# Kernel tuning notes

Hardware: AMD Instinct MI355X
Metric: run time of the kernel (lower is better)

## Reference

```python
import jax, jax.numpy as jnp
import numpy as np

B, T, N, F = 4, 12, 4096, 32
NG = 14  # 14 gate GNNs: fx,fh,ix,ih,cx,ch,ox,oh,i,im,g,gm,o,om


def setup_inputs() -> dict:
    key = jax.random.key(0)
    k1, k2, k3 = jax.random.split(key, 3)
    x = jax.random.normal(k1, (B, T, N, F), dtype=jnp.float32)
    # weighted adjacency, scaled like row-normalized so adj@x stays O(1)
    adj = jax.random.uniform(k2, (B, N, N), dtype=jnp.float32) / N
    W = jax.random.normal(k3, (NG, F, 2 * F), dtype=jnp.float32) * (1.0 / np.sqrt(F))
    b = jnp.zeros((NG, 2 * F), dtype=jnp.float32)
    return {"x": x, "adj": adj, "W": W, "b": b}


def _wgc(v, adj, Wi, bi):
    # WeightedGraphConv: adj-matmul -> Dense(2F) -> GLU
    y = jnp.matmul(adj, v)                 # [B,N,F]
    z = jnp.matmul(y, Wi) + bi             # [B,N,2F]
    ls, rs = jnp.split(z, 2, axis=-1)
    return ls * jax.nn.sigmoid(rs)         # [B,N,F]


def reference(x, adj, W, b):
    Bb, Tt, Nn, Ff = x.shape
    ones = jnp.ones((Bb, Nn, Ff), dtype=x.dtype)
    h0, c0, m0 = ones, ones, ones

    def step(carry, xt):
        h, c, m = carry
        g = lambda i, v: _wgc(v, adj, W[i], b[i])
        f = jax.nn.sigmoid(g(0, xt) + g(1, h))     # forget
        i = jax.nn.sigmoid(g(2, xt) + g(3, h))     # input
        o = jax.nn.sigmoid(g(6, xt) + g(7, h))     # output
        c_new = f * c + i * jnp.tanh(g(4, xt) + g(5, h))
        h_mid = o * jnp.tanh(c_new)
        # memory-state gates (has_memory_state=True)
        i2 = jax.nn.sigmoid(g(8, h_mid) + g(9, m))
        gg = jax.nn.sigmoid(g(10, h_mid) + g(11, m))
        o2 = jax.nn.sigmoid(g(12, h_mid) + g(13, m))
        m_new = i2 * m + (1.0 - i2) * gg
        h_new = m_new * o2
        return (h_new, c_new, m_new), h_new

    (last_h, last_c, last_m), hs = jax.lax.scan(step, (h0, c0, m0), jnp.swapaxes(x, 0, 1))
    hidden_states = jnp.swapaxes(hs, 0, 1)  # [B,T,N,F]
    return hidden_states, last_h, last_c, last_m
```

## Files before the change

kernel.cpp:

```cpp
#include <hip/hip_runtime.h>


typedef __bf16 bf16_t;
typedef __bf16 bf16x8 __attribute__((ext_vector_type(8)));
typedef float  f32x4  __attribute__((ext_vector_type(4)));

#define DI __device__ __forceinline__

#define BB 4
#define TT 12
#define NN 4096
#define FF 32

DI float sigm(float x)  { return __builtin_amdgcn_rcpf(1.f + __expf(-x)); }
DI float tanh_f(float x){ float e = __expf(2.f * x); return 1.f - 2.f * __builtin_amdgcn_rcpf(e + 1.f); }

__global__ __launch_bounds__(256) void conv_adj_k(const float* __restrict__ a,
                                                  bf16_t* __restrict__ o) {
    size_t i = ((size_t)blockIdx.x * 256 + threadIdx.x) * 8;
    float4 v0 = *(const float4*)(a + i);
    float4 v1 = *(const float4*)(a + i + 4);
    union { uint4 u; bf16_t h[8]; } t;
    t.h[0] = (bf16_t)v0.x; t.h[1] = (bf16_t)v0.y; t.h[2] = (bf16_t)v0.z; t.h[3] = (bf16_t)v0.w;
    t.h[4] = (bf16_t)v1.x; t.h[5] = (bf16_t)v1.y; t.h[6] = (bf16_t)v1.z; t.h[7] = (bf16_t)v1.w;
    *(uint4*)(o + i) = t.u;
}

__global__ __launch_bounds__(256) void xpose_k(const float* __restrict__ x,
                                               bf16_t* __restrict__ xT) {
    const int b = blockIdx.z, t = blockIdx.y, n0 = blockIdx.x * 64;
    const int tid = threadIdx.x;
    __shared__ float tile[64][33];
    const float* src = x + (((size_t)(b * TT + t)) * NN + n0) * FF;
#pragma unroll
    for (int rr = 0; rr < 2; ++rr) {
        int idx = rr * 256 + tid;
        int row = idx >> 3, seg = idx & 7;
        float4 v = *(const float4*)(src + row * FF + seg * 4);
        tile[row][seg * 4 + 0] = v.x; tile[row][seg * 4 + 1] = v.y;
        tile[row][seg * 4 + 2] = v.z; tile[row][seg * 4 + 3] = v.w;
    }
    __syncthreads();
    const int f = tid >> 3, seg = tid & 7;
    union { uint4 u; bf16_t h[8]; } o;
#pragma unroll
    for (int j = 0; j < 8; ++j) o.h[j] = (bf16_t)tile[seg * 8 + j][f];
    *(uint4*)&xT[((size_t)(b * 384 + t * FF + f)) * NN + n0 + seg * 8] = o.u;
}

__global__ __launch_bounds__(256) void make_wfrag_k(const float* __restrict__ W,
                                                    bf16_t* __restrict__ Wf) {
    const int g = blockIdx.x, tid = threadIdx.x;
    const int ct = tid >> 6, lane = tid & 63;
    const int k0 = (lane >> 4) * 8, col = ct * 16 + (lane & 15);
    union { uint4 u; bf16_t h[8]; } t;
#pragma unroll
    for (int j = 0; j < 8; ++j) t.h[j] = (bf16_t)W[(g * 32 + k0 + j) * 64 + col];
    *(uint4*)&Wf[((g * 4 + ct) * 64 + lane) * 8] = t.u;
}

__global__ __launch_bounds__(256) void init_k(bf16_t* h_bf, bf16_t* hm_bf,
                                              float* c, float* m,
                                              float* Y1, float* Y2) {
    const int idx = blockIdx.x * 256 + threadIdx.x;
    Y1[idx] = 0.f;
    Y2[idx] = 0.f;
    if (idx < 524288) {
        const int b = idx >> 17, r = idx & 131071;
        h_bf[idx] = (bf16_t)1.f;
        hm_bf[(size_t)b * 262144 + 131072 + r] = (bf16_t)1.f;
        c[idx] = 1.f;
        m[idx] = 1.f;
    }
}

template <bool ABF, int S, int BS0, int BS1>
__global__ __launch_bounds__(256, 4) void gemm_splitk(const void* __restrict__ Ap,
                                                      const bf16_t* __restrict__ p0,
                                                      const bf16_t* __restrict__ p1,
                                                      float* __restrict__ Y) {
    const int b = blockIdx.z;
    const int row0 = blockIdx.x * 64;
    const int slice = blockIdx.y;
    const int tid = threadIdx.x, wave = tid >> 6, lane = tid & 63;
    const int mrow = lane & 15, quad = lane >> 4;
    __shared__ __align__(16) bf16_t Vs[64 * 256];
    const f32x4 zero = {0.f, 0.f, 0.f, 0.f};
    f32x4 acc[4];
#pragma unroll
    for (int i = 0; i < 4; ++i) acc[i] = zero;
    const int row = row0 + wave * 16 + mrow;
    const size_t arow = ((size_t)b << 24) + (size_t)row * NN;

    for (int stg = 0; stg < 4; ++stg) {
        const int k0 = slice * 1024 + stg * 256;
        bf16x8 af[8];
        if constexpr (ABF) {
            const bf16_t* ab = (const bf16_t*)Ap + arow + k0 + quad * 8;
#pragma unroll
            for (int s = 0; s < 8; ++s) af[s] = *(const bf16x8*)(ab + s * 32);
        } else {
            const float* ab = (const float*)Ap + arow + k0 + quad * 8;
#pragma unroll
            for (int s = 0; s < 8; ++s) {
                float4 v0 = *(const float4*)(ab + s * 32);
                float4 v1 = *(const float4*)(ab + s * 32 + 4);
                af[s][0] = (bf16_t)v0.x; af[s][1] = (bf16_t)v0.y;
                af[s][2] = (bf16_t)v0.z; af[s][3] = (bf16_t)v0.w;
                af[s][4] = (bf16_t)v1.x; af[s][5] = (bf16_t)v1.y;
                af[s][6] = (bf16_t)v1.z; af[s][7] = (bf16_t)v1.w;
            }
        }
#pragma unroll
        for (int rr = 0; rr < 8; ++rr) {
            const int idx = rr * 256 + tid;
            const int c = idx >> 5, ch = idx & 31;
            const bf16_t* src = (S < 64 && c >= S)
                ? p1 + ((size_t)b * BS1 + (c - S)) * NN
                : p0 + ((size_t)b * BS0 + c) * NN;
            *(uint4*)&Vs[c * 256 + (ch ^ (c & 7)) * 8] =
                *(const uint4*)(src + k0 + ch * 8);
        }
        __syncthreads();
#pragma unroll
        for (int s = 0; s < 8; ++s) {
#pragma unroll
            for (int ct = 0; ct < 4; ++ct) {
                const int c = ct * 16 + mrow;
                bf16x8 bfr = *(const bf16x8*)&Vs[c * 256 + (((s * 4 + quad) ^ (c & 7)) * 8)];
                acc[ct] = __builtin_amdgcn_mfma_f32_16x16x32_bf16(af[s], bfr, acc[ct], 0, 0, 0);
            }
        }
        __syncthreads();
    }
#pragma unroll
    for (int ct = 0; ct < 4; ++ct) {
        const int col = ct * 16 + mrow;
#pragma unroll
        for (int r = 0; r < 4; ++r) {
            const int orow = row0 + wave * 16 + quad * 4 + r;
            unsafeAtomicAdd(&Y[((size_t)b * NN + orow) * 64 + col], acc[ct][r]);
        }
    }
}

__global__ __launch_bounds__(256) void gates1_k(float* __restrict__ Y1,
                                                const bf16_t* __restrict__ Wf,
                                                const float* __restrict__ bias,
                                                float* __restrict__ c,
                                                bf16_t* __restrict__ hm_bf) {
    const int b = blockIdx.y, n0 = blockIdx.x * 64;
    const int tid = threadIdx.x, wave = tid >> 6, lane = tid & 63;
    const int mrow = lane & 15, quad = lane >> 4;
    const int nw = n0 + wave * 16;
    const f32x4 zero = {0.f, 0.f, 0.f, 0.f};
    float* yr = Y1 + ((size_t)b * NN + nw + mrow) * 64;
    float4 h0 = *(float4*)(yr + quad * 8);
    float4 h1 = *(float4*)(yr + quad * 8 + 4);
    float4 x0 = *(float4*)(yr + 32 + quad * 8);
    float4 x1 = *(float4*)(yr + 32 + quad * 8 + 4);
    const float4 z4 = {0.f, 0.f, 0.f, 0.f};
    *(float4*)(yr + quad * 8) = z4;      *(float4*)(yr + quad * 8 + 4) = z4;
    *(float4*)(yr + 32 + quad * 8) = z4; *(float4*)(yr + 32 + quad * 8 + 4) = z4;
    bf16x8 ah, ax;
    ah[0] = (bf16_t)h0.x; ah[1] = (bf16_t)h0.y; ah[2] = (bf16_t)h0.z; ah[3] = (bf16_t)h0.w;
    ah[4] = (bf16_t)h1.x; ah[5] = (bf16_t)h1.y; ah[6] = (bf16_t)h1.z; ah[7] = (bf16_t)h1.w;
    ax[0] = (bf16_t)x0.x; ax[1] = (bf16_t)x0.y; ax[2] = (bf16_t)x0.z; ax[3] = (bf16_t)x0.w;
    ax[4] = (bf16_t)x1.x; ax[5] = (bf16_t)x1.y; ax[6] = (bf16_t)x1.z; ax[7] = (bf16_t)x1.w;
    float gate[4][2][4];
#pragma unroll
    for (int gi = 0; gi < 4; ++gi) {
        const int ge = 2 * gi, go = ge + 1;
        f32x4 ze[4], zo[4];
#pragma unroll
        for (int ct = 0; ct < 4; ++ct) {
            bf16x8 we = *(const bf16x8*)&Wf[((ge * 4 + ct) * 64 + lane) * 8];
            bf16x8 wo = *(const bf16x8*)&Wf[((go * 4 + ct) * 64 + lane) * 8];
            ze[ct] = __builtin_amdgcn_mfma_f32_16x16x32_bf16(ax, we, zero, 0, 0, 0);
            zo[ct] = __builtin_amdgcn_mfma_f32_16x16x32_bf16(ah, wo, zero, 0, 0, 0);
            const float be = bias[ge * 64 + ct * 16 + mrow];
            const float bo = bias[go * 64 + ct * 16 + mrow];
#pragma unroll
            for (int r = 0; r < 4; ++r) { ze[ct][r] += be; zo[ct][r] += bo; }
        }
#pragma unroll
        for (int p = 0; p < 2; ++p)
#pragma unroll
            for (int r = 0; r < 4; ++r) {
                float s = ze[p][r] * sigm(ze[p + 2][r]) + zo[p][r] * sigm(zo[p + 2][r]);
                gate[gi][p][r] = (gi == 2) ? tanh_f(s) : sigm(s);
            }
    }
    __shared__ bf16_t hmT[32][64];
#pragma unroll
    for (int p = 0; p < 2; ++p)
#pragma unroll
        for (int r = 0; r < 4; ++r) {
            const int row = nw + quad * 4 + r, col = p * 16 + mrow;
            const size_t ci = ((size_t)b * NN + row) * FF + col;
            float cn = gate[0][p][r] * c[ci] + gate[1][p][r] * gate[2][p][r];
            c[ci] = cn;
            hmT[col][wave * 16 + quad * 4 + r] = (bf16_t)(gate[3][p][r] * tanh_f(cn));
        }
    __syncthreads();
    {
        const int col = tid >> 3, seg = tid & 7;
        union { uint4 u; bf16_t h[8]; } o;
#pragma unroll
        for (int j = 0; j < 8; ++j) o.h[j] = hmT[col][seg * 8 + j];
        *(uint4*)&hm_bf[((size_t)b * 64 + col) * NN + n0 + seg * 8] = o.u;
    }
}

__global__ __launch_bounds__(256) void gates2_k(float* __restrict__ Y2,
                                                const bf16_t* __restrict__ Wf,
                                                const float* __restrict__ bias,
                                                float* __restrict__ m,
                                                bf16_t* __restrict__ hm_bf,
                                                bf16_t* __restrict__ h_bf,
                                                float* __restrict__ hs, int t) {
    const int b = blockIdx.y, n0 = blockIdx.x * 64;
    const int tid = threadIdx.x, wave = tid >> 6, lane = tid & 63;
    const int mrow = lane & 15, quad = lane >> 4;
    const int nw = n0 + wave * 16;
    const f32x4 zero = {0.f, 0.f, 0.f, 0.f};
    float* yr = Y2 + ((size_t)b * NN + nw + mrow) * 64;
    float4 h0 = *(float4*)(yr + quad * 8);
    float4 h1 = *(float4*)(yr + quad * 8 + 4);
    float4 m0 = *(float4*)(yr + 32 + quad * 8);
    float4 m1 = *(float4*)(yr + 32 + quad * 8 + 4);
    const float4 z4 = {0.f, 0.f, 0.f, 0.f};
    *(float4*)(yr + quad * 8) = z4;      *(float4*)(yr + quad * 8 + 4) = z4;
    *(float4*)(yr + 32 + quad * 8) = z4; *(float4*)(yr + 32 + quad * 8 + 4) = z4;
    bf16x8 axh, axm;
    axh[0] = (bf16_t)h0.x; axh[1] = (bf16_t)h0.y; axh[2] = (bf16_t)h0.z; axh[3] = (bf16_t)h0.w;
    axh[4] = (bf16_t)h1.x; axh[5] = (bf16_t)h1.y; axh[6] = (bf16_t)h1.z; axh[7] = (bf16_t)h1.w;
    axm[0] = (bf16_t)m0.x; axm[1] = (bf16_t)m0.y; axm[2] = (bf16_t)m0.z; axm[3] = (bf16_t)m0.w;
    axm[4] = (bf16_t)m1.x; axm[5] = (bf16_t)m1.y; axm[6] = (bf16_t)m1.z; axm[7] = (bf16_t)m1.w;
    float gate[3][2][4];
#pragma unroll
    for (int gi = 0; gi < 3; ++gi) {
        const int ge = 8 + 2 * gi, go = ge + 1;
        f32x4 ze[4], zo[4];
#pragma unroll
        for (int ct = 0; ct < 4; ++ct) {
            bf16x8 we = *(const bf16x8*)&Wf[((ge * 4 + ct) * 64 + lane) * 8];
            bf16x8 wo = *(const bf16x8*)&Wf[((go * 4 + ct) * 64 + lane) * 8];
            ze[ct] = __builtin_amdgcn_mfma_f32_16x16x32_bf16(axh, we, zero, 0, 0, 0);
            zo[ct] = __builtin_amdgcn_mfma_f32_16x16x32_bf16(axm, wo, zero, 0, 0, 0);
            const float be = bias[ge * 64 + ct * 16 + mrow];
            const float bo = bias[go * 64 + ct * 16 + mrow];
#pragma unroll
            for (int r = 0; r < 4; ++r) { ze[ct][r] += be; zo[ct][r] += bo; }
        }
#pragma unroll
        for (int p = 0; p < 2; ++p)
#pragma unroll
            for (int r = 0; r < 4; ++r) {
                float s = ze[p][r] * sigm(ze[p + 2][r]) + zo[p][r] * sigm(zo[p + 2][r]);
                gate[gi][p][r] = sigm(s);
            }
    }
    __shared__ bf16_t mT[32][64];
    __shared__ bf16_t hT[32][64];
#pragma unroll
    for (int p = 0; p < 2; ++p)
#pragma unroll
        for (int r = 0; r < 4; ++r) {
            const int row = nw + quad * 4 + r, col = p * 16 + mrow;
            const size_t ci = ((size_t)b * NN + row) * FF + col;
            const float i2 = gate[0][p][r], gg = gate[1][p][r], o2 = gate[2][p][r];
            float mn = i2 * m[ci] + (1.f - i2) * gg;
            m[ci] = mn;
            float hn = mn * o2;
            hs[(((size_t)b * TT + t) * NN + row) * FF + col] = hn;
            mT[col][wave * 16 + quad * 4 + r] = (bf16_t)mn;
            hT[col][wave * 16 + quad * 4 + r] = (bf16_t)hn;
        }
    __syncthreads();
    {
        const int col = tid >> 3, seg = tid & 7;
        union { uint4 u; bf16_t h[8]; } om, oh;
#pragma unroll
        for (int j = 0; j < 8; ++j) { om.h[j] = mT[col][seg * 8 + j]; oh.h[j] = hT[col][seg * 8 + j]; }
        *(uint4*)&hm_bf[((size_t)b * 64 + 32 + col) * NN + n0 + seg * 8] = om.u;
        *(uint4*)&h_bf[((size_t)b * FF + col) * NN + n0 + seg * 8] = oh.u;
    }
}

__global__ __launch_bounds__(256) void finalize_k(const float* __restrict__ hs,
                                                  const float* __restrict__ c,
                                                  const float* __restrict__ m,
                                                  float* __restrict__ tail) {
    const int idx = blockIdx.x * 256 + threadIdx.x;
    const int b = idx >> 17, r = idx & 131071;
    tail[idx] = hs[((size_t)b * TT + (TT - 1)) * 131072 + r];
    tail[524288 + idx] = c[idx];
    tail[1048576 + idx] = m[idx];
}

extern "C" void kernel_launch(void* const* d_in, const int* in_sizes, int n_in,
                              void* d_out, int out_size, void* d_ws, size_t ws_size,
                              hipStream_t stream) {
    const float* x    = (const float*)d_in[0];
    const float* adj  = (const float*)d_in[1];
    const float* W    = (const float*)d_in[2];
    const float* bias = (const float*)d_in[3];
    float* out = (float*)d_out;

    char* ws = (char*)d_ws;
    size_t off = 0;
    auto carve = [&](size_t bytes) -> void* {
        void* p = ws + off;
        off += (bytes + 255) & ~(size_t)255;
        return p;
    };
    bf16_t* xT    = (bf16_t*)carve((size_t)BB * 384 * NN * 2);
    float*  Y1    = (float*)carve((size_t)BB * NN * 64 * 4);
    float*  Y2    = (float*)carve((size_t)BB * NN * 64 * 4);
    bf16_t* h_bf  = (bf16_t*)carve((size_t)BB * FF * NN * 2);
    bf16_t* hm_bf = (bf16_t*)carve((size_t)BB * 64 * NN * 2);
    bf16_t* Wf    = (bf16_t*)carve((size_t)14 * 4 * 64 * 8 * 2);
    float*  cbuf  = (float*)carve((size_t)BB * NN * FF * 4);
    float*  mbuf  = (float*)carve((size_t)BB * NN * FF * 4);
    const size_t adj_bytes = (size_t)BB * NN * NN * 2;
    const bool abf = (ws_size >= off + adj_bytes);
    bf16_t* adj_bf = abf ? (bf16_t*)carve(adj_bytes) : nullptr;

    if (abf) conv_adj_k<<<32768, 256, 0, stream>>>(adj, adj_bf);
    make_wfrag_k<<<14, 256, 0, stream>>>(W, Wf);
    xpose_k<<<dim3(64, TT, BB), 256, 0, stream>>>(x, xT);
    init_k<<<4096, 256, 0, stream>>>(h_bf, hm_bf, cbuf, mbuf, Y1, Y2);

    const dim3 ggrid(64, 4, BB);
    for (int t = 0; t < TT; ++t) {
        const bf16_t* xts = xT + (size_t)t * 32 * NN;
        if (abf) gemm_splitk<true, 32, 32, 384><<<ggrid, 256, 0, stream>>>(adj_bf, h_bf, xts, Y1);
        else     gemm_splitk<false, 32, 32, 384><<<ggrid, 256, 0, stream>>>(adj, h_bf, xts, Y1);
        gates1_k<<<dim3(64, BB), 256, 0, stream>>>(Y1, Wf, bias, cbuf, hm_bf);
        if (abf) gemm_splitk<true, 64, 64, 64><<<ggrid, 256, 0, stream>>>(adj_bf, hm_bf, hm_bf, Y2);
        else     gemm_splitk<false, 64, 64, 64><<<ggrid, 256, 0, stream>>>(adj, hm_bf, hm_bf, Y2);
        gates2_k<<<dim3(64, BB), 256, 0, stream>>>(Y2, Wf, bias, mbuf, hm_bf, h_bf, out, t);
    }
    finalize_k<<<2048, 256, 0, stream>>>(out, cbuf, mbuf, out + (size_t)BB * TT * NN * FF);
}
```

Before: 1.413 ms.

## Replace atomic split-K reduction with per-slice partials and direct global B loads

The split-K GEMM no longer stages the B operand through shared memory with barriers. Each lane now loads its B fragments directly from global memory, and each K-slice writes its partial result to its own buffer instead of issuing atomic adds. The gate kernels sum the four partials on read, so the per-step zeroing of Y and the init-time clears are dropped. The adj conversion also uses nontemporal loads. The trade is 4x larger Y buffers plus extra partial reads, and B fragments that are re-read from global/L2 by every wave rather than shared through LDS.

```diff
diff --git a/kernel.cpp b/kernel.cpp
--- a/kernel.cpp
+++ b/kernel.cpp
@@ -18,11 +18,11 @@
 __global__ __launch_bounds__(256) void conv_adj_k(const float* __restrict__ a,
                                                   bf16_t* __restrict__ o) {
     size_t i = ((size_t)blockIdx.x * 256 + threadIdx.x) * 8;
-    float4 v0 = *(const float4*)(a + i);
-    float4 v1 = *(const float4*)(a + i + 4);
+    f32x4 v0 = __builtin_nontemporal_load((const f32x4*)(a + i));
+    f32x4 v1 = __builtin_nontemporal_load((const f32x4*)(a + i + 4));
     union { uint4 u; bf16_t h[8]; } t;
-    t.h[0] = (bf16_t)v0.x; t.h[1] = (bf16_t)v0.y; t.h[2] = (bf16_t)v0.z; t.h[3] = (bf16_t)v0.w;
-    t.h[4] = (bf16_t)v1.x; t.h[5] = (bf16_t)v1.y; t.h[6] = (bf16_t)v1.z; t.h[7] = (bf16_t)v1.w;
+#pragma unroll
+    for (int j = 0; j < 4; ++j) { t.h[j] = (bf16_t)v0[j]; t.h[4 + j] = (bf16_t)v1[j]; }
     *(uint4*)(o + i) = t.u;
 }
 
@@ -60,91 +60,71 @@
 }
 
 __global__ __launch_bounds__(256) void init_k(bf16_t* h_bf, bf16_t* hm_bf,
-                                              float* c, float* m,
-                                              float* Y1, float* Y2) {
+                                              float* c, float* m) {
     const int idx = blockIdx.x * 256 + threadIdx.x;
-    Y1[idx] = 0.f;
-    Y2[idx] = 0.f;
-    if (idx < 524288) {
-        const int b = idx >> 17, r = idx & 131071;
-        h_bf[idx] = (bf16_t)1.f;
-        hm_bf[(size_t)b * 262144 + 131072 + r] = (bf16_t)1.f;
-        c[idx] = 1.f;
-        m[idx] = 1.f;
-    }
+    const int b = idx >> 17, r = idx & 131071;
+    h_bf[idx] = (bf16_t)1.f;
+    hm_bf[(size_t)b * 262144 + 131072 + r] = (bf16_t)1.f;
+    c[idx] = 1.f;
+    m[idx] = 1.f;
 }
 
 template <bool ABF, int S, int BS0, int BS1>
-__global__ __launch_bounds__(256, 4) void gemm_splitk(const void* __restrict__ Ap,
+__global__ __launch_bounds__(256, 4) void gemm_direct(const void* __restrict__ Ap,
                                                       const bf16_t* __restrict__ p0,
                                                       const bf16_t* __restrict__ p1,
-                                                      float* __restrict__ Y) {
-    const int b = blockIdx.z;
+                                                      float* __restrict__ Yp) {
+    const int b = blockIdx.z, slice = blockIdx.y;
     const int row0 = blockIdx.x * 64;
-    const int slice = blockIdx.y;
     const int tid = threadIdx.x, wave = tid >> 6, lane = tid & 63;
     const int mrow = lane & 15, quad = lane >> 4;
-    __shared__ __align__(16) bf16_t Vs[64 * 256];
-    const f32x4 zero = {0.f, 0.f, 0.f, 0.f};
-    f32x4 acc[4];
-#pragma unroll
-    for (int i = 0; i < 4; ++i) acc[i] = zero;
     const int row = row0 + wave * 16 + mrow;
-    const size_t arow = ((size_t)b << 24) + (size_t)row * NN;
-
-    for (int stg = 0; stg < 4; ++stg) {
-        const int k0 = slice * 1024 + stg * 256;
-        bf16x8 af[8];
-        if constexpr (ABF) {
-            const bf16_t* ab = (const bf16_t*)Ap + arow + k0 + quad * 8;
-#pragma unroll
-            for (int s = 0; s < 8; ++s) af[s] = *(const bf16x8*)(ab + s * 32);
-        } else {
-            const float* ab = (const float*)Ap + arow + k0 + quad * 8;
-#pragma unroll
-            for (int s = 0; s < 8; ++s) {
-                float4 v0 = *(const float4*)(ab + s * 32);
-                float4 v1 = *(const float4*)(ab + s * 32 + 4);
-                af[s][0] = (bf16_t)v0.x; af[s][1] = (bf16_t)v0.y;
-                af[s][2] = (bf16_t)v0.z; af[s][3] = (bf16_t)v0.w;
-                af[s][4] = (bf16_t)v1.x; af[s][5] = (bf16_t)v1.y;
-                af[s][6] = (bf16_t)v1.z; af[s][7] = (bf16_t)v1.w;
-            }
-        }
-#pragma unroll
-        for (int rr = 0; rr < 8; ++rr) {
-            const int idx = rr * 256 + tid;
-            const int c = idx >> 5, ch = idx & 31;
-            const bf16_t* src = (S < 64 && c >= S)
-                ? p1 + ((size_t)b * BS1 + (c - S)) * NN
-                : p0 + ((size_t)b * BS0 + c) * NN;
-            *(uint4*)&Vs[c * 256 + (ch ^ (c & 7)) * 8] =
-                *(const uint4*)(src + k0 + ch * 8);
-        }
-        __syncthreads();
-#pragma unroll
-        for (int s = 0; s < 8; ++s) {
-#pragma unroll
-            for (int ct = 0; ct < 4; ++ct) {
-                const int c = ct * 16 + mrow;
-                bf16x8 bfr = *(const bf16x8*)&Vs[c * 256 + (((s * 4 + quad) ^ (c & 7)) * 8)];
-                acc[ct] = __builtin_amdgcn_mfma_f32_16x16x32_bf16(af[s], bfr, acc[ct], 0, 0, 0);
-            }
-        }
-        __syncthreads();
-    }
+    const int k0 = slice * 1024 + quad * 8;
+    const bf16_t* bp[4];
 #pragma unroll
     for (int ct = 0; ct < 4; ++ct) {
         const int col = ct * 16 + mrow;
-#pragma unroll
-        for (int r = 0; r < 4; ++r) {
-            const int orow = row0 + wave * 16 + quad * 4 + r;
-            unsafeAtomicAdd(&Y[((size_t)b * NN + orow) * 64 + col], acc[ct][r]);
-        }
-    }
-}
-
-__global__ __launch_bounds__(256) void gates1_k(float* __restrict__ Y1,
+        bp[ct] = (ct * 16 < S ? p0 + ((size_t)b * BS0 + col) * NN
+                              : p1 + ((size_t)b * BS1 + (col - S)) * NN) + k0;
+    }
+    const f32x4 zero = {0.f, 0.f, 0.f, 0.f};
+    f32x4 acc[4] = {zero, zero, zero, zero};
+    if constexpr (ABF) {
+        const bf16_t* ap = (const bf16_t*)Ap + ((size_t)b << 24) + (size_t)row * NN + k0;
+#pragma unroll 4
+        for (int kk = 0; kk < 32; ++kk) {
+            bf16x8 af = *(const bf16x8*)(ap + kk * 32);
+#pragma unroll
+            for (int ct = 0; ct < 4; ++ct) {
+                bf16x8 bfr = *(const bf16x8*)(bp[ct] + kk * 32);
+                acc[ct] = __builtin_amdgcn_mfma_f32_16x16x32_bf16(af, bfr, acc[ct], 0, 0, 0);
+            }
+        }
+    } else {
+        const float* ap = (const float*)Ap + ((size_t)b << 24) + (size_t)row * NN + k0;
+#pragma unroll 4
+        for (int kk = 0; kk < 32; ++kk) {
+            f32x4 v0 = *(const f32x4*)(ap + kk * 32);
+            f32x4 v1 = *(const f32x4*)(ap + kk * 32 + 4);
+            bf16x8 af;
+#pragma unroll
+            for (int j = 0; j < 4; ++j) { af[j] = (bf16_t)v0[j]; af[4 + j] = (bf16_t)v1[j]; }
+#pragma unroll
+            for (int ct = 0; ct < 4; ++ct) {
+                bf16x8 bfr = *(const bf16x8*)(bp[ct] + kk * 32);
+                acc[ct] = __builtin_amdgcn_mfma_f32_16x16x32_bf16(af, bfr, acc[ct], 0, 0, 0);
+            }
+        }
+    }
+    float* yb = Yp + (((size_t)b * 4 + slice) * NN + row0 + wave * 16 + quad * 4) * 64 + mrow;
+#pragma unroll
+    for (int ct = 0; ct < 4; ++ct)
+#pragma unroll
+        for (int r = 0; r < 4; ++r)
+            yb[(size_t)r * 64 + ct * 16] = acc[ct][r];
+}
+
+__global__ __launch_bounds__(256) void gates1_k(const float* __restrict__ Y1,
                                                 const bf16_t* __restrict__ Wf,
                                                 const float* __restrict__ bias,
                                                 float* __restrict__ c,
@@ -154,19 +134,22 @@
     const int mrow = lane & 15, quad = lane >> 4;
     const int nw = n0 + wave * 16;
     const f32x4 zero = {0.f, 0.f, 0.f, 0.f};
-    float* yr = Y1 + ((size_t)b * NN + nw + mrow) * 64;
-    float4 h0 = *(float4*)(yr + quad * 8);
-    float4 h1 = *(float4*)(yr + quad * 8 + 4);
-    float4 x0 = *(float4*)(yr + 32 + quad * 8);
-    float4 x1 = *(float4*)(yr + 32 + quad * 8 + 4);
-    const float4 z4 = {0.f, 0.f, 0.f, 0.f};
-    *(float4*)(yr + quad * 8) = z4;      *(float4*)(yr + quad * 8 + 4) = z4;
-    *(float4*)(yr + 32 + quad * 8) = z4; *(float4*)(yr + 32 + quad * 8 + 4) = z4;
+    const float* yr = Y1 + (((size_t)b * 4) * NN + nw + mrow) * 64 + quad * 8;
+    f32x4 h0 = zero, h1 = zero, x0 = zero, x1 = zero;
+#pragma unroll
+    for (int s = 0; s < 4; ++s) {
+        const float* p = yr + (size_t)s * NN * 64;
+        h0 += *(const f32x4*)(p);
+        h1 += *(const f32x4*)(p + 4);
+        x0 += *(const f32x4*)(p + 32);
+        x1 += *(const f32x4*)(p + 36);
+    }
     bf16x8 ah, ax;
-    ah[0] = (bf16_t)h0.x; ah[1] = (bf16_t)h0.y; ah[2] = (bf16_t)h0.z; ah[3] = (bf16_t)h0.w;
-    ah[4] = (bf16_t)h1.x; ah[5] = (bf16_t)h1.y; ah[6] = (bf16_t)h1.z; ah[7] = (bf16_t)h1.w;
-    ax[0] = (bf16_t)x0.x; ax[1] = (bf16_t)x0.y; ax[2] = (bf16_t)x0.z; ax[3] = (bf16_t)x0.w;
-    ax[4] = (bf16_t)x1.x; ax[5] = (bf16_t)x1.y; ax[6] = (bf16_t)x1.z; ax[7] = (bf16_t)x1.w;
+#pragma unroll
+    for (int j = 0; j < 4; ++j) {
+        ah[j] = (bf16_t)h0[j]; ah[4 + j] = (bf16_t)h1[j];
+        ax[j] = (bf16_t)x0[j]; ax[4 + j] = (bf16_t)x1[j];
+    }
     float gate[4][2][4];
 #pragma unroll
     for (int gi = 0; gi < 4; ++gi) {
@@ -212,7 +195,7 @@
     }
 }
 
-__global__ __launch_bounds__(256) void gates2_k(float* __restrict__ Y2,
+__global__ __launch_bounds__(256) void gates2_k(const float* __restrict__ Y2,
                                                 const bf16_t* __restrict__ Wf,
                                                 const float* __restrict__ bias,
                                                 float* __restrict__ m,
@@ -224,19 +207,22 @@
     const int mrow = lane & 15, quad = lane >> 4;
     const int nw = n0 + wave * 16;
     const f32x4 zero = {0.f, 0.f, 0.f, 0.f};
-    float* yr = Y2 + ((size_t)b * NN + nw + mrow) * 64;
-    float4 h0 = *(float4*)(yr + quad * 8);
-    float4 h1 = *(float4*)(yr + quad * 8 + 4);
-    float4 m0 = *(float4*)(yr + 32 + quad * 8);
-    float4 m1 = *(float4*)(yr + 32 + quad * 8 + 4);
-    const float4 z4 = {0.f, 0.f, 0.f, 0.f};
-    *(float4*)(yr + quad * 8) = z4;      *(float4*)(yr + quad * 8 + 4) = z4;
-    *(float4*)(yr + 32 + quad * 8) = z4; *(float4*)(yr + 32 + quad * 8 + 4) = z4;
+    const float* yr = Y2 + (((size_t)b * 4) * NN + nw + mrow) * 64 + quad * 8;
+    f32x4 h0 = zero, h1 = zero, m0 = zero, m1 = zero;
+#pragma unroll
+    for (int s = 0; s < 4; ++s) {
+        const float* p = yr + (size_t)s * NN * 64;
+        h0 += *(const f32x4*)(p);
+        h1 += *(const f32x4*)(p + 4);
+        m0 += *(const f32x4*)(p + 32);
+        m1 += *(const f32x4*)(p + 36);
+    }
     bf16x8 axh, axm;
-    axh[0] = (bf16_t)h0.x; axh[1] = (bf16_t)h0.y; axh[2] = (bf16_t)h0.z; axh[3] = (bf16_t)h0.w;
-    axh[4] = (bf16_t)h1.x; axh[5] = (bf16_t)h1.y; axh[6] = (bf16_t)h1.z; axh[7] = (bf16_t)h1.w;
-    axm[0] = (bf16_t)m0.x; axm[1] = (bf16_t)m0.y; axm[2] = (bf16_t)m0.z; axm[3] = (bf16_t)m0.w;
-    axm[4] = (bf16_t)m1.x; axm[5] = (bf16_t)m1.y; axm[6] = (bf16_t)m1.z; axm[7] = (bf16_t)m1.w;
+#pragma unroll
+    for (int j = 0; j < 4; ++j) {
+        axh[j] = (bf16_t)h0[j]; axh[4 + j] = (bf16_t)h1[j];
+        axm[j] = (bf16_t)m0[j]; axm[4 + j] = (bf16_t)m1[j];
+    }
     float gate[3][2][4];
 #pragma unroll
     for (int gi = 0; gi < 3; ++gi) {
@@ -316,8 +302,8 @@
         return p;
     };
     bf16_t* xT    = (bf16_t*)carve((size_t)BB * 384 * NN * 2);
-    float*  Y1    = (float*)carve((size_t)BB * NN * 64 * 4);
-    float*  Y2    = (float*)carve((size_t)BB * NN * 64 * 4);
+    float*  Y1    = (float*)carve((size_t)BB * 4 * NN * 64 * 4);
+    float*  Y2    = (float*)carve((size_t)BB * 4 * NN * 64 * 4);
     bf16_t* h_bf  = (bf16_t*)carve((size_t)BB * FF * NN * 2);
     bf16_t* hm_bf = (bf16_t*)carve((size_t)BB * 64 * NN * 2);
     bf16_t* Wf    = (bf16_t*)carve((size_t)14 * 4 * 64 * 8 * 2);
@@ -330,16 +316,16 @@
     if (abf) conv_adj_k<<<32768, 256, 0, stream>>>(adj, adj_bf);
     make_wfrag_k<<<14, 256, 0, stream>>>(W, Wf);
     xpose_k<<<dim3(64, TT, BB), 256, 0, stream>>>(x, xT);
-    init_k<<<4096, 256, 0, stream>>>(h_bf, hm_bf, cbuf, mbuf, Y1, Y2);
+    init_k<<<2048, 256, 0, stream>>>(h_bf, hm_bf, cbuf, mbuf);
 
     const dim3 ggrid(64, 4, BB);
     for (int t = 0; t < TT; ++t) {
         const bf16_t* xts = xT + (size_t)t * 32 * NN;
-        if (abf) gemm_splitk<true, 32, 32, 384><<<ggrid, 256, 0, stream>>>(adj_bf, h_bf, xts, Y1);
-        else     gemm_splitk<false, 32, 32, 384><<<ggrid, 256, 0, stream>>>(adj, h_bf, xts, Y1);
+        if (abf) gemm_direct<true, 32, 32, 384><<<ggrid, 256, 0, stream>>>(adj_bf, h_bf, xts, Y1);
+        else     gemm_direct<false, 32, 32, 384><<<ggrid, 256, 0, stream>>>(adj, h_bf, xts, Y1);
         gates1_k<<<dim3(64, BB), 256, 0, stream>>>(Y1, Wf, bias, cbuf, hm_bf);
-        if (abf) gemm_splitk<true, 64, 64, 64><<<ggrid, 256, 0, stream>>>(adj_bf, hm_bf, hm_bf, Y2);
-        else     gemm_splitk<false, 64, 64, 64><<<ggrid, 256, 0, stream>>>(adj, hm_bf, hm_bf, Y2);
+        if (abf) gemm_direct<true, 64, 64, 64><<<ggrid, 256, 0, stream>>>(adj_bf, hm_bf, hm_bf, Y2);
+        else     gemm_direct<false, 64, 64, 64><<<ggrid, 256, 0, stream>>>(adj, hm_bf, hm_bf, Y2);
         gates2_k<<<dim3(64, BB), 256, 0, stream>>>(Y2, Wf, bias, mbuf, hm_bf, h_bf, out, t);
     }
     finalize_k<<<2048, 256, 0, stream>>>(out, cbuf, mbuf, out + (size_t)BB * TT * NN * FF);
```

After: 2.343 ms. 65.8% more time.
